# Performance work log

Measured on AMD Instinct MI355X. Metric: run time of the kernel, lower is better.

## Reference

```python
import jax, jax.numpy as jnp
import numpy as np

N_NODES = 50000


def _gcn_conv(x, edge_index, W, b, num_nodes):
    """PyG GCNConv: h = D^{-1/2} (A + I) D^{-1/2} (x W) + b."""
    # add self loops
    loops = jnp.arange(num_nodes, dtype=edge_index.dtype)
    src = jnp.concatenate([edge_index[0], loops])  # [E + N]
    dst = jnp.concatenate([edge_index[1], loops])
    # symmetric degree normalization (edge weight 1.0, incl. self loops)
    deg = jax.ops.segment_sum(jnp.ones_like(src, dtype=x.dtype), dst,
                              num_segments=num_nodes)
    dinv = jnp.where(deg > 0, jax.lax.rsqrt(deg), 0.0)
    norm = dinv[src] * dinv[dst]  # [E + N]
    h = x @ W  # [N, H] dense GEMM first (PyG applies lin before propagate)
    msgs = h[src] * norm[:, None]  # gather + scale, [E + N, H]
    out = jax.ops.segment_sum(msgs, dst, num_segments=num_nodes)  # scatter-add
    return out + b


def setup_inputs() -> dict:
    key = jax.random.key(0)
    ks = jax.random.split(key, 6)
    F_in, H = 100, 1024
    state = jax.random.normal(ks[0], (N_NODES, F_in, 1), dtype=jnp.float32)
    edge_index = jax.random.randint(ks[1], (2, 200000), 0, N_NODES, dtype=jnp.int64)
    W1 = jax.random.normal(ks[2], (F_in, H), dtype=jnp.float32) / np.sqrt(F_in)
    b1 = jax.random.normal(ks[3], (H,), dtype=jnp.float32) * 0.01
    W_head = jax.random.normal(ks[4], (H, 1), dtype=jnp.float32) / np.sqrt(H)
    b_head = jax.random.normal(ks[5], (1,), dtype=jnp.float32) * 0.01
    return {"state": state, "edge_index": edge_index, "W1": W1, "b1": b1,
            "W_head": W_head, "b_head": b_head}


def reference(state, edge_index, W1, b1, W_head, b_head):
    x = state.reshape(state.shape[0], state.shape[1])  # (N, F, 1) -> (N, F)
    h = _gcn_conv(x, edge_index, W1, b1, N_NODES)      # GCNConv 100 -> 1024
    return h @ W_head + b_head                          # linear head -> (N, 1)
```

## Files before the change

kernel.cpp:

```cpp
#include <hip/hip_runtime.h>


#define N_NODES 50000
#define F_IN    100
#define H_DIM   1024
#define N_EDGES 200000

__global__ void __launch_bounds__(256)
k0_zero_fold(const float* __restrict__ W1, const float* __restrict__ b1,
             const float* __restrict__ Wh, const float* __restrict__ bh,
             float* __restrict__ w, float* __restrict__ c,
             float4* __restrict__ zero_region)
{
    const int b = blockIdx.x;
    const int t = threadIdx.x;
    if (b <= 100) {
        const float* row = (b < 100) ? (W1 + (size_t)b * H_DIM) : b1;
        float s = 0.0f;
        #pragma unroll
        for (int k = 0; k < H_DIM / 256; ++k) {
            const int h = t + 256 * k;
            s += row[h] * Wh[h];
        }
        #pragma unroll
        for (int off = 32; off > 0; off >>= 1) s += __shfl_down(s, off, 64);
        __shared__ float red[4];
        const int wave = t >> 6, lane = t & 63;
        if (lane == 0) red[wave] = s;
        __syncthreads();
        if (t == 0) {
            const float tot = red[0] + red[1] + red[2] + red[3];
            if (b < 100) w[b] = tot;
            else         *c  = tot + bh[0];
        }
    } else {
        const int g = (b - 101) * 256 + t;
        if (g < (2 * N_NODES) / 4)
            zero_region[g] = make_float4(0.f, 0.f, 0.f, 0.f);
    }
}

__global__ void __launch_bounds__(256)
k1_deg_score(const float* __restrict__ x, const int* __restrict__ ei,
             const float* __restrict__ w,
             unsigned* __restrict__ deg, float* __restrict__ sbuf)
{
    const int tid   = blockIdx.x * 256 + threadIdx.x;
    const int gwave = tid >> 6;
    const int lane  = tid & 63;

    if (tid < N_EDGES / 4) {
        const int4 d4 = ((const int4*)(ei + N_EDGES))[tid];
        atomicAdd(&deg[d4.x], 1u);
        atomicAdd(&deg[d4.y], 1u);
        atomicAdd(&deg[d4.z], 1u);
        atomicAdd(&deg[d4.w], 1u);
    }

    if (gwave < N_NODES) {
        const float* row = x + (size_t)gwave * F_IN;
        float s = row[lane] * w[lane];
        if (lane < F_IN - 64) s += row[64 + lane] * w[64 + lane];
        #pragma unroll
        for (int off = 32; off > 0; off >>= 1) s += __shfl_down(s, off, 64);
        if (lane == 0) sbuf[gwave] = s;
    }
}

__global__ void __launch_bounds__(256)
k2_scatter(const int* __restrict__ ei, const unsigned* __restrict__ deg,
           const float* __restrict__ sbuf, float* __restrict__ acc)
{
    const int g = blockIdx.x * 256 + threadIdx.x;
    if (g >= N_EDGES / 2) return;
    const int2 s2 = ((const int2*)ei)[g];
    const int2 d2 = ((const int2*)(ei + N_EDGES))[g];
    const float u0 = sbuf[s2.x] * rsqrtf((float)deg[s2.x] + 1.0f);
    const float u1 = sbuf[s2.y] * rsqrtf((float)deg[s2.y] + 1.0f);
    unsafeAtomicAdd(&acc[d2.x], u0);
    unsafeAtomicAdd(&acc[d2.y], u1);
}

__global__ void __launch_bounds__(256)
k3_final(const uint4* __restrict__ deg4, const float4* __restrict__ acc4,
         const float4* __restrict__ s4, const float* __restrict__ c,
         float4* __restrict__ out4)
{
    const int g = blockIdx.x * 256 + threadIdx.x;
    if (g >= N_NODES / 4) return;
    const uint4  d = deg4[g];
    const float4 a = acc4[g];
    const float4 s = s4[g];
    const float  cv = c[0];
    float4 o;
    float dv;
    dv  = rsqrtf((float)d.x + 1.0f); o.x = dv * a.x + dv * dv * s.x + cv;
    dv  = rsqrtf((float)d.y + 1.0f); o.y = dv * a.y + dv * dv * s.y + cv;
    dv  = rsqrtf((float)d.z + 1.0f); o.z = dv * a.z + dv * dv * s.z + cv;
    dv  = rsqrtf((float)d.w + 1.0f); o.w = dv * a.w + dv * dv * s.w + cv;
    out4[g] = o;
}

extern "C" void kernel_launch(void* const* d_in, const int* in_sizes, int n_in,
                              void* d_out, int out_size, void* d_ws, size_t ws_size,
                              hipStream_t stream)
{
    const float* x   = (const float*)d_in[0];
    const int*   ei  = (const int*)  d_in[1];
    const float* W1  = (const float*)d_in[2];
    const float* b1  = (const float*)d_in[3];
    const float* Wh  = (const float*)d_in[4];
    const float* bh  = (const float*)d_in[5];
    float*       out = (float*)d_out;

    float*    ws_f = (float*)d_ws;
    float*    w    = ws_f;
    float*    c    = ws_f + 100;
    unsigned* deg  = (unsigned*)(ws_f + 128);
    float*    acc  = ws_f + 128 + N_NODES;
    float*    sbuf = ws_f + 128 + 2 * N_NODES;

    k0_zero_fold<<<199, 256, 0, stream>>>(W1, b1, Wh, bh, w, c, (float4*)deg);
    k1_deg_score<<<(N_NODES * 64 + 255) / 256, 256, 0, stream>>>(x, ei, w, deg, sbuf);
    k2_scatter<<<(N_EDGES / 2 + 255) / 256, 256, 0, stream>>>(ei, deg, sbuf, acc);
    k3_final<<<(N_NODES / 4 + 255) / 256, 256, 0, stream>>>(
        (const uint4*)deg, (const float4*)acc, (const float4*)sbuf, c, (float4*)out);
}
```

Measured before the change: 103.5 us.

## Fold final normalization into scatter kernel, dropping separate finalize pass

Removes the fourth kernel by seeding the output with the folded bias in the degree kernel and having the scatter kernel atomically add fully normalized edge messages and self-loop terms directly into the output. This eliminates one launch and the intermediate accumulator buffer read/write. In exchange, each edge computes an extra rsqrt and gathers the destination degree, and self-loop contributions become extra atomics.

```diff
diff --git a/kernel.cpp b/kernel.cpp
--- a/kernel.cpp
+++ b/kernel.cpp
@@ -7,10 +7,10 @@
 #define N_EDGES 200000
 
 __global__ void __launch_bounds__(256)
-k0_zero_fold(const float* __restrict__ W1, const float* __restrict__ b1,
+k0_fold_zero(const float* __restrict__ W1, const float* __restrict__ b1,
              const float* __restrict__ Wh, const float* __restrict__ bh,
              float* __restrict__ w, float* __restrict__ c,
-             float4* __restrict__ zero_region)
+             float4* __restrict__ deg_zero)
 {
     const int b = blockIdx.x;
     const int t = threadIdx.x;
@@ -35,15 +35,16 @@
         }
     } else {
         const int g = (b - 101) * 256 + t;
-        if (g < (2 * N_NODES) / 4)
-            zero_region[g] = make_float4(0.f, 0.f, 0.f, 0.f);
+        if (g < N_NODES / 4)
+            deg_zero[g] = make_float4(0.f, 0.f, 0.f, 0.f);
     }
 }
 
 __global__ void __launch_bounds__(256)
-k1_deg_score(const float* __restrict__ x, const int* __restrict__ ei,
-             const float* __restrict__ w,
-             unsigned* __restrict__ deg, float* __restrict__ sbuf)
+k1_deg_seed_score(const float* __restrict__ x, const int* __restrict__ ei,
+                  const float* __restrict__ w, const float* __restrict__ c,
+                  unsigned* __restrict__ deg, float* __restrict__ sbuf,
+                  float4* __restrict__ out4)
 {
     const int tid   = blockIdx.x * 256 + threadIdx.x;
     const int gwave = tid >> 6;
@@ -55,6 +56,9 @@
         atomicAdd(&deg[d4.y], 1u);
         atomicAdd(&deg[d4.z], 1u);
         atomicAdd(&deg[d4.w], 1u);
+    } else if (tid < N_EDGES / 4 + N_NODES / 4) {
+        const float cv = c[0];
+        out4[tid - N_EDGES / 4] = make_float4(cv, cv, cv, cv);
     }
 
     if (gwave < N_NODES) {
@@ -69,36 +73,23 @@
 
 __global__ void __launch_bounds__(256)
 k2_scatter(const int* __restrict__ ei, const unsigned* __restrict__ deg,
-           const float* __restrict__ sbuf, float* __restrict__ acc)
+           const float* __restrict__ sbuf, float* __restrict__ out)
 {
-    const int g = blockIdx.x * 256 + threadIdx.x;
-    if (g >= N_EDGES / 2) return;
-    const int2 s2 = ((const int2*)ei)[g];
-    const int2 d2 = ((const int2*)(ei + N_EDGES))[g];
-    const float u0 = sbuf[s2.x] * rsqrtf((float)deg[s2.x] + 1.0f);
-    const float u1 = sbuf[s2.y] * rsqrtf((float)deg[s2.y] + 1.0f);
-    unsafeAtomicAdd(&acc[d2.x], u0);
-    unsafeAtomicAdd(&acc[d2.y], u1);
-}
-
-__global__ void __launch_bounds__(256)
-k3_final(const uint4* __restrict__ deg4, const float4* __restrict__ acc4,
-         const float4* __restrict__ s4, const float* __restrict__ c,
-         float4* __restrict__ out4)
-{
-    const int g = blockIdx.x * 256 + threadIdx.x;
-    if (g >= N_NODES / 4) return;
-    const uint4  d = deg4[g];
-    const float4 a = acc4[g];
-    const float4 s = s4[g];
-    const float  cv = c[0];
-    float4 o;
-    float dv;
-    dv  = rsqrtf((float)d.x + 1.0f); o.x = dv * a.x + dv * dv * s.x + cv;
-    dv  = rsqrtf((float)d.y + 1.0f); o.y = dv * a.y + dv * dv * s.y + cv;
-    dv  = rsqrtf((float)d.z + 1.0f); o.z = dv * a.z + dv * dv * s.z + cv;
-    dv  = rsqrtf((float)d.w + 1.0f); o.w = dv * a.w + dv * dv * s.w + cv;
-    out4[g] = o;
+    const int tid = blockIdx.x * 256 + threadIdx.x;
+    if (tid < N_EDGES / 2) {
+        const int2 s2 = ((const int2*)ei)[tid];
+        const int2 d2 = ((const int2*)(ei + N_EDGES))[tid];
+        const float u0 = sbuf[s2.x] * rsqrtf((float)deg[s2.x] + 1.0f)
+                                    * rsqrtf((float)deg[d2.x] + 1.0f);
+        const float u1 = sbuf[s2.y] * rsqrtf((float)deg[s2.y] + 1.0f)
+                                    * rsqrtf((float)deg[d2.y] + 1.0f);
+        unsafeAtomicAdd(&out[d2.x], u0);
+        unsafeAtomicAdd(&out[d2.y], u1);
+    } else if (tid < N_EDGES / 2 + N_NODES) {
+        const int i = tid - N_EDGES / 2;
+        const float dv = rsqrtf((float)deg[i] + 1.0f);
+        unsafeAtomicAdd(&out[i], dv * dv * sbuf[i]);
+    }
 }
 
 extern "C" void kernel_launch(void* const* d_in, const int* in_sizes, int n_in,
@@ -117,12 +108,12 @@
     float*    w    = ws_f;
     float*    c    = ws_f + 100;
     unsigned* deg  = (unsigned*)(ws_f + 128);
-    float*    acc  = ws_f + 128 + N_NODES;
-    float*    sbuf = ws_f + 128 + 2 * N_NODES;
+    float*    sbuf = ws_f + 128 + N_NODES;
 
-    k0_zero_fold<<<199, 256, 0, stream>>>(W1, b1, Wh, bh, w, c, (float4*)deg);
-    k1_deg_score<<<(N_NODES * 64 + 255) / 256, 256, 0, stream>>>(x, ei, w, deg, sbuf);
-    k2_scatter<<<(N_EDGES / 2 + 255) / 256, 256, 0, stream>>>(ei, deg, sbuf, acc);
-    k3_final<<<(N_NODES / 4 + 255) / 256, 256, 0, stream>>>(
-        (const uint4*)deg, (const float4*)acc, (const float4*)sbuf, c, (float4*)out);
+    k0_fold_zero<<<101 + (N_NODES / 4 + 255) / 256, 256, 0, stream>>>(
+        W1, b1, Wh, bh, w, c, (float4*)deg);
+    k1_deg_seed_score<<<(N_NODES * 64 + 255) / 256, 256, 0, stream>>>(
+        x, ei, w, c, deg, sbuf, (float4*)out);
+    k2_scatter<<<(N_EDGES / 2 + N_NODES + 255) / 256, 256, 0, stream>>>(
+        ei, deg, sbuf, out);
 }
```

New measurement: 102.9 us, median of 2. Within noise of the previous version (-0.6%).
